# Kernel tuning notes

Measured on AMD Instinct MI355X. Metric: run time of the kernel, lower is better.

Reference implementation:

```python
import jax, jax.numpy as jnp
import numpy as np

# Irrep dims for irreps 0e, 1o, 2e: 2l+1
IRREP_DIMS = (1, 3, 5)
B, N, C_IN, C_OUT = 8, 4096, 256, 256
FEAT = sum(IRREP_DIMS)  # 9


def setup_inputs() -> dict:
    key = jax.random.key(0)
    kx, k0, k1, k2 = jax.random.split(key, 4)
    std = C_IN ** -0.5  # VarianceScaling(fan_in) init
    return {
        "x": jax.random.normal(kx, (B, N, C_IN, FEAT), dtype=jnp.float32),
        "w0": jax.random.normal(k0, (C_IN, C_OUT), dtype=jnp.float32) * std,
        "w1": jax.random.normal(k1, (C_IN, C_OUT), dtype=jnp.float32) * std,
        "w2": jax.random.normal(k2, (C_IN, C_OUT), dtype=jnp.float32) * std,
    }


def reference(x, w0, w1, w2):
    # EquivariantLinear with mix_channels=True:
    #  - axis_to_mul merges the channel axis into irrep multiplicity, so each
    #    irrep block x[..., k, m] (k = channel/mul index, m = 2l+1 component)
    #    is contracted over k with a per-irrep weight w_l [mul_in, mul_out],
    #    scaled by path_weight = 1/sqrt(fan_in) (single path per output irrep).
    #  - mul_to_axis splits the multiplicity back into the channel axis.
    # Block-diagonal structure: one small matmul per matching irrep pair.
    mul_in = x.shape[-2]
    pw = jnp.asarray(mul_in, x.dtype) ** -0.5  # path_weight (1/sqrt fan_in)
    outs = []
    offset = 0
    for w, d in zip((w0, w1, w2), IRREP_DIMS):
        xl = jax.lax.slice_in_dim(x, offset, offset + d, axis=-1)  # [B,N,C,d]
        outs.append(pw * jnp.einsum('bnkm,kc->bncm', xl, w))
        offset += d
    return jnp.concatenate(outs, axis=-1)  # [B, N, C_out, 9]
```

## Files before the change

### kernel.cpp

```cpp
#include <hip/hip_runtime.h>


typedef float f32x4 __attribute__((ext_vector_type(4)));
typedef float f32x4u __attribute__((ext_vector_type(4), aligned(4)));
typedef short s16x8 __attribute__((ext_vector_type(8)));

#define POSB 16
#define XS_KS 264
#define XS_MS (POSB * XS_KS)
#define BUF_BYTES (9 * XS_MS * 2)
#define SMEM_BYTES (2 * BUF_BYTES)
#define STG_ROW 148
#define NT 4
#define TILE_FLOATS (POSB * 2304)

__device__ __forceinline__ unsigned short f2bf(float f) {
  unsigned u = __float_as_uint(f);
  return (unsigned short)((u + 0x7FFFu + ((u >> 16) & 1u)) >> 16);
}

__device__ __forceinline__ unsigned cvt_pk_bf16(float lo, float hi) {
  unsigned r;
  asm("v_cvt_pk_bf16_f32 %0, %1, %2" : "=v"(r) : "v"(lo), "v"(hi));
  return r;
}

__device__ __forceinline__ void bar_nodrain() {
  asm volatile("s_waitcnt lgkmcnt(0)\n\ts_barrier" ::: "memory");
}

__global__ void prep_w(const float* __restrict__ w0, const float* __restrict__ w1,
                       const float* __restrict__ w2, unsigned short* __restrict__ wt) {
  const int b = blockIdx.x;
  const int irr = b / 16;
  const int tile = b % 16;
  const int k0 = (tile >> 2) << 6;
  const int c0 = (tile & 3) << 6;
  const float* w = (irr == 0) ? w0 : ((irr == 1) ? w1 : w2);
  __shared__ float lt[64 * 65];
  const int t = threadIdx.x;
#pragma unroll
  for (int i = 0; i < 16; ++i) {
    int e = t + (i << 8);
    int kk = e >> 6, cc = e & 63;
    lt[cc * 65 + kk] = w[(k0 + kk) * 256 + (c0 + cc)];
  }
  __syncthreads();
#pragma unroll
  for (int i = 0; i < 16; ++i) {
    int e = t + (i << 8);
    int cc = e >> 6, kk = e & 63;
    wt[irr * 65536 + (c0 + cc) * 256 + (k0 + kk)] = f2bf(lt[cc * 65 + kk] * 0.0625f);
  }
}

__device__ __forceinline__ void load8(const float* __restrict__ xb, int t,
                                      f32x4u* va, f32x4u* vb, float* vc) {
#pragma unroll
  for (int i = 0; i < 8; ++i) {
    const float* s = xb + (t + (i << 9)) * 9;
    va[i] = *reinterpret_cast<const f32x4u*>(s);
    vb[i] = *reinterpret_cast<const f32x4u*>(s + 4);
    vc[i] = s[8];
  }
}

__device__ __forceinline__ void stage8(unsigned short* __restrict__ xs, int t,
                                       const f32x4u* va, const f32x4u* vb,
                                       const float* vc) {
#pragma unroll
  for (int i = 0; i < 8; ++i) {
    const int u = t + (i << 9);
    const int pos = u >> 8;
    const int k = u & 255;
    unsigned short* base = xs + pos * XS_KS + k;
    unsigned p01 = cvt_pk_bf16(va[i][0], va[i][1]);
    unsigned p23 = cvt_pk_bf16(va[i][2], va[i][3]);
    unsigned p45 = cvt_pk_bf16(vb[i][0], vb[i][1]);
    unsigned p67 = cvt_pk_bf16(vb[i][2], vb[i][3]);
    base[0 * XS_MS] = (unsigned short)p01;
    base[1 * XS_MS] = (unsigned short)(p01 >> 16);
    base[2 * XS_MS] = (unsigned short)p23;
    base[3 * XS_MS] = (unsigned short)(p23 >> 16);
    base[4 * XS_MS] = (unsigned short)p45;
    base[5 * XS_MS] = (unsigned short)(p45 >> 16);
    base[6 * XS_MS] = (unsigned short)p67;
    base[7 * XS_MS] = (unsigned short)(p67 >> 16);
    base[8 * XS_MS] = f2bf(vc[i]);
  }
}

__global__ __launch_bounds__(512, 2) void eqlin_main(
    const float* __restrict__ x, const unsigned short* __restrict__ wt,
    float* __restrict__ out) {
  extern __shared__ char smem[];

  const int t = threadIdx.x;
  const long long blk = blockIdx.x;
  const float* xbase = x + blk * (NT * TILE_FLOATS);

  const int w = t >> 6;
  const int l = t & 63;
  const int cr = l & 15;
  const int kg = (l >> 4) << 3;
  const int c0 = w << 5;
  const unsigned short* wtB = wt + (c0 + cr) * 256 + kg;

  f32x4u va[8], vb[8];
  float vc[8];

  load8(xbase, t, va, vb, vc);
  stage8(reinterpret_cast<unsigned short*>(smem), t, va, vb, vc);
  bar_nodrain();

#pragma unroll 2
  for (int it = 0; it < NT; ++it) {
    const int p = it & 1;
    const unsigned short* xsb =
        reinterpret_cast<const unsigned short*>(smem + p * BUF_BYTES);

    if (it + 1 < NT) load8(xbase + (it + 1) * TILE_FLOATS, t, va, vb, vc);

    const unsigned short* xsA = xsb + cr * XS_KS + kg;

    f32x4 accA[4][2];
#pragma unroll
    for (int m = 0; m < 4; ++m)
#pragma unroll
      for (int ct = 0; ct < 2; ++ct) accA[m][ct] = (f32x4){0.f, 0.f, 0.f, 0.f};

#pragma unroll 2
    for (int ks = 0; ks < 8; ++ks) {
      const int kk = ks << 5;
      s16x8 b00 = *reinterpret_cast<const s16x8*>(wtB + kk);
      s16x8 b01 = *reinterpret_cast<const s16x8*>(wtB + 4096 + kk);
      s16x8 b10 = *reinterpret_cast<const s16x8*>(wtB + 65536 + kk);
      s16x8 b11 = *reinterpret_cast<const s16x8*>(wtB + 65536 + 4096 + kk);
      {
        s16x8 a = *reinterpret_cast<const s16x8*>(xsA + kk);
        accA[0][0] = __builtin_amdgcn_mfma_f32_16x16x32_bf16(a, b00, accA[0][0], 0, 0, 0);
        accA[0][1] = __builtin_amdgcn_mfma_f32_16x16x32_bf16(a, b01, accA[0][1], 0, 0, 0);
      }
#pragma unroll
      for (int m = 1; m < 4; ++m) {
        s16x8 a = *reinterpret_cast<const s16x8*>(xsA + m * XS_MS + kk);
        accA[m][0] = __builtin_amdgcn_mfma_f32_16x16x32_bf16(a, b10, accA[m][0], 0, 0, 0);
        accA[m][1] = __builtin_amdgcn_mfma_f32_16x16x32_bf16(a, b11, accA[m][1], 0, 0, 0);
      }
    }

    f32x4 accB[5][2];
#pragma unroll
    for (int m = 0; m < 5; ++m)
#pragma unroll
      for (int ct = 0; ct < 2; ++ct) accB[m][ct] = (f32x4){0.f, 0.f, 0.f, 0.f};

#pragma unroll 2
    for (int ks = 0; ks < 8; ++ks) {
      const int kk = ks << 5;
      s16x8 b20 = *reinterpret_cast<const s16x8*>(wtB + 2 * 65536 + kk);
      s16x8 b21 = *reinterpret_cast<const s16x8*>(wtB + 2 * 65536 + 4096 + kk);
#pragma unroll
      for (int m = 0; m < 5; ++m) {
        s16x8 a = *reinterpret_cast<const s16x8*>(xsA + (m + 4) * XS_MS + kk);
        accB[m][0] = __builtin_amdgcn_mfma_f32_16x16x32_bf16(a, b20, accB[m][0], 0, 0, 0);
        accB[m][1] = __builtin_amdgcn_mfma_f32_16x16x32_bf16(a, b21, accB[m][1], 0, 0, 0);
      }
    }
    bar_nodrain();

    float* stgw = reinterpret_cast<float*>(smem + p * BUF_BYTES) + w * (POSB * STG_ROW);
    const int posb = (l >> 4) << 2;
    f32x4* o4 = reinterpret_cast<f32x4*>(out) + (blk * NT + it) * 9216 + w * 72;

#pragma unroll
    for (int ct = 0; ct < 2; ++ct) {
#pragma unroll
      for (int m = 0; m < 9; ++m) {
#pragma unroll
        for (int j = 0; j < 4; ++j) {
          float v = (m < 4) ? accA[m][ct][j] : accB[m - 4][ct][j];
          stgw[(posb + j) * STG_ROW + cr * 9 + m] = v;
        }
      }
      asm volatile("s_waitcnt lgkmcnt(0)" ::: "memory");
#pragma unroll
      for (int q = 0; q < 9; ++q) {
        const int e = l + (q << 6);
        const int pos = (int)((unsigned)e / 36u);
        const int rem = e - pos * 36;
        f32x4 v = *reinterpret_cast<const f32x4*>(stgw + pos * STG_ROW + (rem << 2));
        __builtin_nontemporal_store(v, &o4[pos * 576 + ct * 36 + rem]);
      }
      asm volatile("s_waitcnt lgkmcnt(0)" ::: "memory");
    }

    if (it + 1 < NT) {
      stage8(reinterpret_cast<unsigned short*>(smem + (p ^ 1) * BUF_BYTES), t, va, vb, vc);
    }
    bar_nodrain();
  }
}

extern "C" void kernel_launch(void* const* d_in, const int* in_sizes, int n_in,
                              void* d_out, int out_size, void* d_ws, size_t ws_size,
                              hipStream_t stream) {
  const float* x = (const float*)d_in[0];
  const float* w0 = (const float*)d_in[1];
  const float* w1 = (const float*)d_in[2];
  const float* w2 = (const float*)d_in[3];
  unsigned short* wt = (unsigned short*)d_ws;
  float* out = (float*)d_out;

  prep_w<<<48, 256, 0, stream>>>(w0, w1, w2, wt);

  (void)hipFuncSetAttribute(reinterpret_cast<const void*>(eqlin_main),
                            hipFuncAttributeMaxDynamicSharedMemorySize, SMEM_BYTES);
  eqlin_main<<<512, 512, SMEM_BYTES, stream>>>(x, wt, out);
}
```

Measured before the change: 192.4 us.

## Single-buffer LDS tile and raise occupancy to four blocks per CU

Drops the LDS double buffer, halving shared memory per block, and raises launch bounds from 2 to 4 blocks per CU. The next tile's global load now starts late, during the output store phase, instead of overlapping the MFMA compute. This trades intra-block prefetch overlap for inter-block overlap from higher occupancy. Register pressure at 4x512 threads may cause spills, and the extra barriers serialize staging.

New measurement: 285.3 us. 48.3% more time.

```diff
diff --git a/kernel.cpp b/kernel.cpp
--- a/kernel.cpp
+++ b/kernel.cpp
@@ -8,8 +8,7 @@
 #define POSB 16
 #define XS_KS 264
 #define XS_MS (POSB * XS_KS)
-#define BUF_BYTES (9 * XS_MS * 2)
-#define SMEM_BYTES (2 * BUF_BYTES)
+#define SMEM_BYTES (9 * XS_MS * 2)
 #define STG_ROW 148
 #define NT 4
 #define TILE_FLOATS (POSB * 2304)
@@ -90,14 +89,15 @@
   }
 }
 
-__global__ __launch_bounds__(512, 2) void eqlin_main(
+__global__ __launch_bounds__(512, 4) void eqlin_main(
     const float* __restrict__ x, const unsigned short* __restrict__ wt,
     float* __restrict__ out) {
   extern __shared__ char smem[];
+  unsigned short* xs = reinterpret_cast<unsigned short*>(smem);
 
   const int t = threadIdx.x;
   const long long blk = blockIdx.x;
-  const float* xbase = x + blk * (NT * TILE_FLOATS);
+  const float* xbase = x + blk * ((long long)NT * TILE_FLOATS);
 
   const int w = t >> 6;
   const int l = t & 63;
@@ -106,22 +106,19 @@
   const int c0 = w << 5;
   const unsigned short* wtB = wt + (c0 + cr) * 256 + kg;
 
+  float* stgw = reinterpret_cast<float*>(smem) + w * (POSB * STG_ROW);
+  const int posb = (l >> 4) << 2;
+
   f32x4u va[8], vb[8];
   float vc[8];
 
   load8(xbase, t, va, vb, vc);
-  stage8(reinterpret_cast<unsigned short*>(smem), t, va, vb, vc);
+  stage8(xs, t, va, vb, vc);
   bar_nodrain();
 
-#pragma unroll 2
+#pragma unroll 1
   for (int it = 0; it < NT; ++it) {
-    const int p = it & 1;
-    const unsigned short* xsb =
-        reinterpret_cast<const unsigned short*>(smem + p * BUF_BYTES);
-
-    if (it + 1 < NT) load8(xbase + (it + 1) * TILE_FLOATS, t, va, vb, vc);
-
-    const unsigned short* xsA = xsb + cr * XS_KS + kg;
+    const unsigned short* xsA = xs + cr * XS_KS + kg;
 
     f32x4 accA[4][2];
 #pragma unroll
@@ -169,36 +166,51 @@
     }
     bar_nodrain();
 
-    float* stgw = reinterpret_cast<float*>(smem + p * BUF_BYTES) + w * (POSB * STG_ROW);
-    const int posb = (l >> 4) << 2;
     f32x4* o4 = reinterpret_cast<f32x4*>(out) + (blk * NT + it) * 9216 + w * 72;
 
 #pragma unroll
-    for (int ct = 0; ct < 2; ++ct) {
-#pragma unroll
-      for (int m = 0; m < 9; ++m) {
-#pragma unroll
-        for (int j = 0; j < 4; ++j) {
-          float v = (m < 4) ? accA[m][ct][j] : accB[m - 4][ct][j];
-          stgw[(posb + j) * STG_ROW + cr * 9 + m] = v;
-        }
-      }
-      asm volatile("s_waitcnt lgkmcnt(0)" ::: "memory");
-#pragma unroll
-      for (int q = 0; q < 9; ++q) {
-        const int e = l + (q << 6);
-        const int pos = (int)((unsigned)e / 36u);
-        const int rem = e - pos * 36;
-        f32x4 v = *reinterpret_cast<const f32x4*>(stgw + pos * STG_ROW + (rem << 2));
-        __builtin_nontemporal_store(v, &o4[pos * 576 + ct * 36 + rem]);
-      }
-      asm volatile("s_waitcnt lgkmcnt(0)" ::: "memory");
+    for (int m = 0; m < 9; ++m)
+#pragma unroll
+      for (int j = 0; j < 4; ++j) {
+        float v = (m < 4) ? accA[m][0][j] : accB[m - 4][0][j];
+        stgw[(posb + j) * STG_ROW + cr * 9 + m] = v;
+      }
+    asm volatile("s_waitcnt lgkmcnt(0)" ::: "memory");
+#pragma unroll
+    for (int q = 0; q < 9; ++q) {
+      const int e = l + (q << 6);
+      const int pos = (int)((unsigned)e / 36u);
+      const int rem = e - pos * 36;
+      f32x4 v = *reinterpret_cast<const f32x4*>(stgw + pos * STG_ROW + (rem << 2));
+      __builtin_nontemporal_store(v, &o4[pos * 576 + rem]);
+    }
+    asm volatile("s_waitcnt lgkmcnt(0)" ::: "memory");
+
+#pragma unroll
+    for (int m = 0; m < 9; ++m)
+#pragma unroll
+      for (int j = 0; j < 4; ++j) {
+        float v = (m < 4) ? accA[m][1][j] : accB[m - 4][1][j];
+        stgw[(posb + j) * STG_ROW + cr * 9 + m] = v;
+      }
+    asm volatile("s_waitcnt lgkmcnt(0)" ::: "memory");
+
+    if (it + 1 < NT) load8(xbase + (long long)(it + 1) * TILE_FLOATS, t, va, vb, vc);
+
+#pragma unroll
+    for (int q = 0; q < 9; ++q) {
+      const int e = l + (q << 6);
+      const int pos = (int)((unsigned)e / 36u);
+      const int rem = e - pos * 36;
+      f32x4 v = *reinterpret_cast<const f32x4*>(stgw + pos * STG_ROW + (rem << 2));
+      __builtin_nontemporal_store(v, &o4[pos * 576 + 36 + rem]);
     }
 
     if (it + 1 < NT) {
-      stage8(reinterpret_cast<unsigned short*>(smem + (p ^ 1) * BUF_BYTES), t, va, vb, vc);
-    }
-    bar_nodrain();
+      bar_nodrain();
+      stage8(xs, t, va, vb, vc);
+      bar_nodrain();
+    }
   }
 }
 
```

## Split block into producer and MFMA consumer waves with direct output stores

Applied to the files above, without the earlier changes.

Warp-specializes the block: four waves load x from global memory, convert it to bf16 and stage it into double-buffered LDS, while the other four waves run the MFMA matmuls over all 64 output channels each and write results straight to global memory. The LDS staging transpose for the output is dropped, and each block now processes eight tiles with half as many blocks launched. The goal is to overlap loads with compute and cut LDS traffic, at the cost of uncoalesced 9-float strided output stores, more accumulator registers per compute wave, and only half the waves issuing MFMAs.

New measurement: 345.5 us. 79.6% more time.

```diff
diff --git a/kernel.cpp b/kernel.cpp
--- a/kernel.cpp
+++ b/kernel.cpp
@@ -10,8 +10,7 @@
 #define XS_MS (POSB * XS_KS)
 #define BUF_BYTES (9 * XS_MS * 2)
 #define SMEM_BYTES (2 * BUF_BYTES)
-#define STG_ROW 148
-#define NT 4
+#define NT 8
 #define TILE_FLOATS (POSB * 2304)
 
 __device__ __forceinline__ unsigned short f2bf(float f) {
@@ -54,26 +53,21 @@
   }
 }
 
-__device__ __forceinline__ void load8(const float* __restrict__ xb, int t,
-                                      f32x4u* va, f32x4u* vb, float* vc) {
+__device__ __forceinline__ void stage_chunk(const float* __restrict__ xb,
+                                            unsigned short* __restrict__ xs,
+                                            int tp, int i0) {
+  f32x4u va[8], vb[8];
+  float vc[8];
 #pragma unroll
   for (int i = 0; i < 8; ++i) {
-    const float* s = xb + (t + (i << 9)) * 9;
+    const float* s = xb + (((i0 + i) << 8) + tp) * 9;
     va[i] = *reinterpret_cast<const f32x4u*>(s);
     vb[i] = *reinterpret_cast<const f32x4u*>(s + 4);
     vc[i] = s[8];
   }
-}
-
-__device__ __forceinline__ void stage8(unsigned short* __restrict__ xs, int t,
-                                       const f32x4u* va, const f32x4u* vb,
-                                       const float* vc) {
 #pragma unroll
   for (int i = 0; i < 8; ++i) {
-    const int u = t + (i << 9);
-    const int pos = u >> 8;
-    const int k = u & 255;
-    unsigned short* base = xs + pos * XS_KS + k;
+    unsigned short* base = xs + (i0 + i) * XS_KS + tp;
     unsigned p01 = cvt_pk_bf16(va[i][0], va[i][1]);
     unsigned p23 = cvt_pk_bf16(va[i][2], va[i][3]);
     unsigned p45 = cvt_pk_bf16(vb[i][0], vb[i][1]);
@@ -97,108 +91,109 @@
 
   const int t = threadIdx.x;
   const long long blk = blockIdx.x;
-  const float* xbase = x + blk * (NT * TILE_FLOATS);
-
+  const float* xbase = x + blk * ((long long)NT * TILE_FLOATS);
   const int w = t >> 6;
-  const int l = t & 63;
-  const int cr = l & 15;
-  const int kg = (l >> 4) << 3;
-  const int c0 = w << 5;
-  const unsigned short* wtB = wt + (c0 + cr) * 256 + kg;
-
-  f32x4u va[8], vb[8];
-  float vc[8];
-
-  load8(xbase, t, va, vb, vc);
-  stage8(reinterpret_cast<unsigned short*>(smem), t, va, vb, vc);
-  bar_nodrain();
+
+  if (w < 4) {
+    const int tp = t;
+    unsigned short* buf0 = reinterpret_cast<unsigned short*>(smem);
+    stage_chunk(xbase, buf0, tp, 0);
+    stage_chunk(xbase, buf0, tp, 8);
+    bar_nodrain();
+#pragma unroll 1
+    for (int it = 0; it < NT; ++it) {
+      if (it + 1 < NT) {
+        const float* xb = xbase + (long long)(it + 1) * TILE_FLOATS;
+        unsigned short* bn =
+            reinterpret_cast<unsigned short*>(smem + ((it + 1) & 1) * BUF_BYTES);
+        stage_chunk(xb, bn, tp, 0);
+        stage_chunk(xb, bn, tp, 8);
+      }
+      bar_nodrain();
+    }
+  } else {
+    const int wv = w - 4;
+    const int l = t & 63;
+    const int cr = l & 15;
+    const int g = l >> 4;
+    const int kg = g << 3;
+    const int c0 = wv << 6;
+    const unsigned short* wtB = wt + (c0 + cr) * 256 + kg;
+
+    bar_nodrain();
+#pragma unroll 1
+    for (int it = 0; it < NT; ++it) {
+      const unsigned short* xsb =
+          reinterpret_cast<const unsigned short*>(smem + (it & 1) * BUF_BYTES);
+      const unsigned short* xsA = xsb + cr * XS_KS + kg;
+
+      f32x4 accA[4][4];
+#pragma unroll
+      for (int m = 0; m < 4; ++m)
+#pragma unroll
+        for (int ct = 0; ct < 4; ++ct) accA[m][ct] = (f32x4){0.f, 0.f, 0.f, 0.f};
 
 #pragma unroll 2
-  for (int it = 0; it < NT; ++it) {
-    const int p = it & 1;
-    const unsigned short* xsb =
-        reinterpret_cast<const unsigned short*>(smem + p * BUF_BYTES);
-
-    if (it + 1 < NT) load8(xbase + (it + 1) * TILE_FLOATS, t, va, vb, vc);
-
-    const unsigned short* xsA = xsb + cr * XS_KS + kg;
-
-    f32x4 accA[4][2];
-#pragma unroll
-    for (int m = 0; m < 4; ++m)
-#pragma unroll
-      for (int ct = 0; ct < 2; ++ct) accA[m][ct] = (f32x4){0.f, 0.f, 0.f, 0.f};
+      for (int ks = 0; ks < 8; ++ks) {
+        const int kk = ks << 5;
+        s16x8 a0 = *reinterpret_cast<const s16x8*>(xsA + kk);
+        s16x8 a1 = *reinterpret_cast<const s16x8*>(xsA + 1 * XS_MS + kk);
+        s16x8 a2 = *reinterpret_cast<const s16x8*>(xsA + 2 * XS_MS + kk);
+        s16x8 a3 = *reinterpret_cast<const s16x8*>(xsA + 3 * XS_MS + kk);
+#pragma unroll
+        for (int ct = 0; ct < 4; ++ct) {
+          const unsigned short* wc = wtB + ct * 4096 + kk;
+          s16x8 b0 = *reinterpret_cast<const s16x8*>(wc);
+          s16x8 b1 = *reinterpret_cast<const s16x8*>(wc + 65536);
+          accA[0][ct] = __builtin_amdgcn_mfma_f32_16x16x32_bf16(a0, b0, accA[0][ct], 0, 0, 0);
+          accA[1][ct] = __builtin_amdgcn_mfma_f32_16x16x32_bf16(a1, b1, accA[1][ct], 0, 0, 0);
+          accA[2][ct] = __builtin_amdgcn_mfma_f32_16x16x32_bf16(a2, b1, accA[2][ct], 0, 0, 0);
+          accA[3][ct] = __builtin_amdgcn_mfma_f32_16x16x32_bf16(a3, b1, accA[3][ct], 0, 0, 0);
+        }
+      }
+
+      f32x4 accB[5][4];
+#pragma unroll
+      for (int m = 0; m < 5; ++m)
+#pragma unroll
+        for (int ct = 0; ct < 4; ++ct) accB[m][ct] = (f32x4){0.f, 0.f, 0.f, 0.f};
 
 #pragma unroll 2
-    for (int ks = 0; ks < 8; ++ks) {
-      const int kk = ks << 5;
-      s16x8 b00 = *reinterpret_cast<const s16x8*>(wtB + kk);
-      s16x8 b01 = *reinterpret_cast<const s16x8*>(wtB + 4096 + kk);
-      s16x8 b10 = *reinterpret_cast<const s16x8*>(wtB + 65536 + kk);
-      s16x8 b11 = *reinterpret_cast<const s16x8*>(wtB + 65536 + 4096 + kk);
-      {
-        s16x8 a = *reinterpret_cast<const s16x8*>(xsA + kk);
-        accA[0][0] = __builtin_amdgcn_mfma_f32_16x16x32_bf16(a, b00, accA[0][0], 0, 0, 0);
-        accA[0][1] = __builtin_amdgcn_mfma_f32_16x16x32_bf16(a, b01, accA[0][1], 0, 0, 0);
-      }
-#pragma unroll
-      for (int m = 1; m < 4; ++m) {
-        s16x8 a = *reinterpret_cast<const s16x8*>(xsA + m * XS_MS + kk);
-        accA[m][0] = __builtin_amdgcn_mfma_f32_16x16x32_bf16(a, b10, accA[m][0], 0, 0, 0);
-        accA[m][1] = __builtin_amdgcn_mfma_f32_16x16x32_bf16(a, b11, accA[m][1], 0, 0, 0);
-      }
+      for (int ks = 0; ks < 8; ++ks) {
+        const int kk = ks << 5;
+        s16x8 a4 = *reinterpret_cast<const s16x8*>(xsA + 4 * XS_MS + kk);
+        s16x8 a5 = *reinterpret_cast<const s16x8*>(xsA + 5 * XS_MS + kk);
+        s16x8 a6 = *reinterpret_cast<const s16x8*>(xsA + 6 * XS_MS + kk);
+        s16x8 a7 = *reinterpret_cast<const s16x8*>(xsA + 7 * XS_MS + kk);
+        s16x8 a8 = *reinterpret_cast<const s16x8*>(xsA + 8 * XS_MS + kk);
+#pragma unroll
+        for (int ct = 0; ct < 4; ++ct) {
+          const unsigned short* wc = wtB + ct * 4096 + kk;
+          s16x8 b2 = *reinterpret_cast<const s16x8*>(wc + 131072);
+          accB[0][ct] = __builtin_amdgcn_mfma_f32_16x16x32_bf16(a4, b2, accB[0][ct], 0, 0, 0);
+          accB[1][ct] = __builtin_amdgcn_mfma_f32_16x16x32_bf16(a5, b2, accB[1][ct], 0, 0, 0);
+          accB[2][ct] = __builtin_amdgcn_mfma_f32_16x16x32_bf16(a6, b2, accB[2][ct], 0, 0, 0);
+          accB[3][ct] = __builtin_amdgcn_mfma_f32_16x16x32_bf16(a7, b2, accB[3][ct], 0, 0, 0);
+          accB[4][ct] = __builtin_amdgcn_mfma_f32_16x16x32_bf16(a8, b2, accB[4][ct], 0, 0, 0);
+        }
+      }
+
+      const long long obase = (long long)(blk * NT + it) * TILE_FLOATS;
+#pragma unroll
+      for (int ct = 0; ct < 4; ++ct) {
+        const int c = c0 + (ct << 4) + cr;
+#pragma unroll
+        for (int j = 0; j < 4; ++j) {
+          float* o = out + obase + (((g << 2) + j) * 256 + c) * 9;
+          f32x4u v0 = {accA[0][ct][j], accA[1][ct][j], accA[2][ct][j], accA[3][ct][j]};
+          f32x4u v1 = {accB[0][ct][j], accB[1][ct][j], accB[2][ct][j], accB[3][ct][j]};
+          __builtin_nontemporal_store(v0, reinterpret_cast<f32x4u*>(o));
+          __builtin_nontemporal_store(v1, reinterpret_cast<f32x4u*>(o + 4));
+          __builtin_nontemporal_store(accB[4][ct][j], o + 8);
+        }
+      }
+      bar_nodrain();
     }
-
-    f32x4 accB[5][2];
-#pragma unroll
-    for (int m = 0; m < 5; ++m)
-#pragma unroll
-      for (int ct = 0; ct < 2; ++ct) accB[m][ct] = (f32x4){0.f, 0.f, 0.f, 0.f};
-
-#pragma unroll 2
-    for (int ks = 0; ks < 8; ++ks) {
-      const int kk = ks << 5;
-      s16x8 b20 = *reinterpret_cast<const s16x8*>(wtB + 2 * 65536 + kk);
-      s16x8 b21 = *reinterpret_cast<const s16x8*>(wtB + 2 * 65536 + 4096 + kk);
-#pragma unroll
-      for (int m = 0; m < 5; ++m) {
-        s16x8 a = *reinterpret_cast<const s16x8*>(xsA + (m + 4) * XS_MS + kk);
-        accB[m][0] = __builtin_amdgcn_mfma_f32_16x16x32_bf16(a, b20, accB[m][0], 0, 0, 0);
-        accB[m][1] = __builtin_amdgcn_mfma_f32_16x16x32_bf16(a, b21, accB[m][1], 0, 0, 0);
-      }
-    }
-    bar_nodrain();
-
-    float* stgw = reinterpret_cast<float*>(smem + p * BUF_BYTES) + w * (POSB * STG_ROW);
-    const int posb = (l >> 4) << 2;
-    f32x4* o4 = reinterpret_cast<f32x4*>(out) + (blk * NT + it) * 9216 + w * 72;
-
-#pragma unroll
-    for (int ct = 0; ct < 2; ++ct) {
-#pragma unroll
-      for (int m = 0; m < 9; ++m) {
-#pragma unroll
-        for (int j = 0; j < 4; ++j) {
-          float v = (m < 4) ? accA[m][ct][j] : accB[m - 4][ct][j];
-          stgw[(posb + j) * STG_ROW + cr * 9 + m] = v;
-        }
-      }
-      asm volatile("s_waitcnt lgkmcnt(0)" ::: "memory");
-#pragma unroll
-      for (int q = 0; q < 9; ++q) {
-        const int e = l + (q << 6);
-        const int pos = (int)((unsigned)e / 36u);
-        const int rem = e - pos * 36;
-        f32x4 v = *reinterpret_cast<const f32x4*>(stgw + pos * STG_ROW + (rem << 2));
-        __builtin_nontemporal_store(v, &o4[pos * 576 + ct * 36 + rem]);
-      }
-      asm volatile("s_waitcnt lgkmcnt(0)" ::: "memory");
-    }
-
-    if (it + 1 < NT) {
-      stage8(reinterpret_cast<unsigned short*>(smem + (p ^ 1) * BUF_BYTES), t, va, vb, vc);
-    }
-    bar_nodrain();
   }
 }
 
@@ -216,5 +211,5 @@
 
   (void)hipFuncSetAttribute(reinterpret_cast<const void*>(eqlin_main),
                             hipFuncAttributeMaxDynamicSharedMemorySize, SMEM_BYTES);
-  eqlin_main<<<512, 512, SMEM_BYTES, stream>>>(x, wt, out);
-}
+  eqlin_main<<<256, 512, SMEM_BYTES, stream>>>(x, wt, out);
+}
```
